# Kernel optimization log

Measured on AMD Instinct MI355X. Metric: run time of the kernel, lower is better.

Reference implementation:

```python
import jax, jax.numpy as jnp
import numpy as np

B, N, C = 4, 2048, 768
H = 12
D = C // H  # head_dim = 64
SCALE = D ** -0.5


def setup_inputs() -> dict:
    key = jax.random.key(0)
    ks = jax.random.split(key, 9)
    x = jax.random.normal(ks[0], (B, N, C), dtype=jnp.float32)
    k_in = jax.random.normal(ks[1], (B, N, C), dtype=jnp.float32)
    v_in = jax.random.normal(ks[2], (B, N, C), dtype=jnp.float32)
    rel_pos_bias = jax.random.normal(ks[3], (H, N, N), dtype=jnp.float32)
    # learned params (nn.Linear stores weight [out, in]; y = x @ W.T + b)
    s = C ** -0.5
    Wq = jax.random.normal(ks[4], (C, C), dtype=jnp.float32) * s
    Wk = jax.random.normal(ks[5], (C, C), dtype=jnp.float32) * s
    Wv = jax.random.normal(ks[6], (C, C), dtype=jnp.float32) * s
    Wp = jax.random.normal(ks[7], (C, C), dtype=jnp.float32) * s
    bp = jax.random.normal(ks[8], (C,), dtype=jnp.float32) * 0.01
    return {"x": x, "k_in": k_in, "v_in": v_in, "rel_pos_bias": rel_pos_bias,
            "Wq": Wq, "Wk": Wk, "Wv": Wv, "Wp": Wp, "bp": bp}


def reference(x, k_in, v_in, rel_pos_bias, Wq, Wk, Wv, Wp, bp):
    # linear projections (no q/k/v bias since qkv_bias=False)
    q = jnp.einsum('bnc,dc->bnd', x, Wq)      # [B,N,C]
    k = jnp.einsum('bnc,dc->bnd', k_in, Wk)   # [B,Nk,C]
    v = jnp.einsum('bnc,dc->bnd', v_in, Wv)   # [B,Nv,C]
    # split heads -> [B,H,N,D]
    q = q.reshape(B, N, H, D).transpose(0, 2, 1, 3) * SCALE
    k = k.reshape(B, -1, H, D).transpose(0, 2, 1, 3)
    v = v.reshape(B, -1, H, D).transpose(0, 2, 1, 3)
    attn = jnp.einsum('bhnd,bhmd->bhnm', q, k)          # [B,H,N,Nk]
    attn = attn + rel_pos_bias[None]                    # additive rel-pos bias
    attn = jax.nn.softmax(attn, axis=-1)
    out = jnp.einsum('bhnm,bhmd->bhnd', attn, v)        # [B,H,N,D]
    out = out.transpose(0, 2, 1, 3).reshape(B, N, C)
    return jnp.einsum('bnc,dc->bnd', out, Wp) + bp
```

## Files before the change

### kernel.cpp

```cpp
#include <hip/hip_runtime.h>
#include <stdint.h>
#include <stddef.h>

#define B_ 4
#define N_ 2048
#define C_ 768
#define H_ 12
#define M_ (B_ * N_)

typedef __attribute__((ext_vector_type(8))) short bf16x8_t;
typedef __attribute__((ext_vector_type(4))) float f32x4_t;

__device__ __forceinline__ unsigned pack2_bf16(float f0, float f1) {
  unsigned u0 = __builtin_bit_cast(unsigned, f0) + 0x8000u;
  unsigned u1 = __builtin_bit_cast(unsigned, f1) + 0x8000u;
  return __builtin_amdgcn_perm(u1, u0, 0x07060302u);
}

__device__ __forceinline__ short f2bf(float f) {
  unsigned u = __builtin_bit_cast(unsigned, f);
  u = (u + 0x7FFFu + ((u >> 16) & 1u)) >> 16;
  return (short)u;
}
__device__ __forceinline__ short f2bf_fast(float f) {
  return (short)((__builtin_bit_cast(unsigned, f) + 0x8000u) >> 16);
}

__device__ __forceinline__ void gload_lds16(const short* g, const short* l) {
  __builtin_amdgcn_global_load_lds(
      (const __attribute__((address_space(1))) void*)g,
      (__attribute__((address_space(3))) void*)l, 16, 0, 0);
}

#define XV 1572864
#define WV 147456
__global__ __launch_bounds__(256) void cvt_all(
    const float* __restrict__ x, const float* __restrict__ kin, const float* __restrict__ vin,
    const float* __restrict__ wq, const float* __restrict__ wk, const float* __restrict__ wv,
    const float* __restrict__ wp,
    unsigned short* __restrict__ xb, unsigned short* __restrict__ kb, unsigned short* __restrict__ vb,
    unsigned short* __restrict__ wqb, unsigned short* __restrict__ wkb, unsigned short* __restrict__ wvb,
    unsigned short* __restrict__ wpb)
{
  int i = blockIdx.x * 256 + threadIdx.x;
  const float* s; unsigned short* d; int off;
  if      (i < XV)            { s = x;   d = xb;  off = i; }
  else if (i < 2 * XV)        { s = kin; d = kb;  off = i - XV; }
  else if (i < 3 * XV)        { s = vin; d = vb;  off = i - 2 * XV; }
  else if (i < 3 * XV + WV)   { s = wq;  d = wqb; off = i - 3 * XV; }
  else if (i < 3 * XV + 2*WV) { s = wk;  d = wkb; off = i - 3 * XV - WV; }
  else if (i < 3 * XV + 3*WV) { s = wv;  d = wvb; off = i - 3 * XV - 2 * WV; }
  else                        { s = wp;  d = wpb; off = i - 3 * XV - 3 * WV; }
  float4 v = ((const float4*)s)[off];
  uint2 p;
  p.x = pack2_bf16(v.x, v.y);
  p.y = pack2_bf16(v.z, v.w);
  ((uint2*)d)[off] = p;
}

__global__ __launch_bounds__(256) void proj_qkv(
    const short* __restrict__ xb, const short* __restrict__ kb, const short* __restrict__ vb,
    const short* __restrict__ wqb, const short* __restrict__ wkb, const short* __restrict__ wvb,
    short* __restrict__ q_ws, short* __restrict__ k_ws, short* __restrict__ vt_ws)
{
  const int z = blockIdx.z;
  const short* A = (z == 0) ? xb : (z == 1) ? kb : vb;
  const short* W = (z == 0) ? wqb : (z == 1) ? wkb : wvb;
  const int m0 = blockIdx.x * 128;
  const int n0 = blockIdx.y * 128;

  __shared__ __align__(16) short smem[128 * 136];
  short* As = smem;
  short* Bs = smem + 128 * 64;

  const int t = threadIdx.x;
  const int w = t >> 6, L = t & 63, L15 = L & 15, quad = L >> 4;
  const int wm = w & 1, wn = w >> 1;

  f32x4_t acc[4][4] = {};

  const short* ga = A + (size_t)(m0 + w * 32 + (L >> 3)) * C_ + (L & 7) * 8;
  const short* gb = W + (size_t)(n0 + w * 32 + (L >> 3)) * C_ + (L & 7) * 8;
  const short* la = As + (w * 32) * 64;
  const short* lb = Bs + (w * 32) * 64;

  for (int k0 = 0; k0 < C_; k0 += 64) {
    __syncthreads();
    #pragma unroll
    for (int i = 0; i < 4; ++i) {
      gload_lds16(ga + (size_t)i * 8 * C_ + k0, la + i * 512);
      gload_lds16(gb + (size_t)i * 8 * C_ + k0, lb + i * 512);
    }
    __syncthreads();
    #pragma unroll
    for (int kk = 0; kk < 2; ++kk) {
      bf16x8_t af[4], bf[4];
      #pragma unroll
      for (int mt = 0; mt < 4; ++mt)
        af[mt] = *(const bf16x8_t*)&As[(wm * 64 + mt * 16 + L15) * 64 + kk * 32 + quad * 8];
      #pragma unroll
      for (int nt = 0; nt < 4; ++nt)
        bf[nt] = *(const bf16x8_t*)&Bs[(wn * 64 + nt * 16 + L15) * 64 + kk * 32 + quad * 8];
      #pragma unroll
      for (int mt = 0; mt < 4; ++mt)
        #pragma unroll
        for (int nt = 0; nt < 4; ++nt)
          acc[mt][nt] = __builtin_amdgcn_mfma_f32_16x16x32_bf16(af[mt], bf[nt], acc[mt][nt], 0, 0, 0);
    }
  }

  if (z != 2) {
    short* outp = (z == 0) ? q_ws : k_ws;
    const float mul = (z == 0) ? 0.125f : 1.0f;
    #pragma unroll
    for (int mt = 0; mt < 4; ++mt) {
      const int m_base = m0 + wm * 64 + mt * 16 + quad * 4;
      #pragma unroll
      for (int nt = 0; nt < 4; ++nt) {
        const int c = n0 + wn * 64 + nt * 16 + L15;
        const int h = c >> 6, d = c & 63;
        #pragma unroll
        for (int r = 0; r < 4; ++r) {
          const int m = m_base + r;
          const int b = m >> 11, n = m & 2047;
          outp[((size_t)(b * H_ + h) * N_ + n) * 64 + d] = f2bf(acc[mt][nt][r] * mul);
        }
      }
    }
  } else {
    __syncthreads();
    #pragma unroll
    for (int mt = 0; mt < 4; ++mt) {
      const int ml = wm * 64 + mt * 16 + quad * 4;
      #pragma unroll
      for (int nt = 0; nt < 4; ++nt) {
        const int cl = wn * 64 + nt * 16 + L15;
        #pragma unroll
        for (int r = 0; r < 4; ++r)
          smem[cl * 136 + ml + r] = f2bf(acc[mt][nt][r]);
      }
    }
    __syncthreads();
    const int bb = m0 >> 11;
    const int nn0 = m0 & 2047;
    #pragma unroll
    for (int pp = 0; pp < 8; ++pp) {
      const int cl = pp * 16 + (t >> 4);
      const int mg = t & 15;
      const uint4 val = *(const uint4*)&smem[cl * 136 + mg * 8];
      const int cg = n0 + cl;
      *(uint4*)&vt_ws[(((size_t)(bb * H_ + (cg >> 6))) * 64 + (cg & 63)) * N_ + nn0 + mg * 8] = val;
    }
  }
}

__global__ __launch_bounds__(256, 3) void attn(
    const short* __restrict__ q_ws, const short* __restrict__ k_ws,
    const short* __restrict__ vt_ws, const float* __restrict__ rpb,
    short* __restrict__ attn_out)
{
  const int p  = blockIdx.x;
  const int lw = (p & 7) * 96 + (p >> 3);
  const int h  = lw >> 6;
  const int xl = lw & 63;
  const int b  = xl & 3;
  const int m0 = (xl >> 2) * 128;
  const int bh = b * H_ + h;

  __shared__ __align__(16) short Ks [2][64 * 64];
  __shared__ __align__(16) short Vts[2][64 * 64];
  __shared__ __align__(16) short Ps [4][32 * 64];

  const int t = threadIdx.x;
  const int w = t >> 6, L = t & 63, L15 = L & 15, quad = L >> 4;

  const short* qp  = q_ws  + ((size_t)bh * N_ + m0) * 64;
  const short* kp  = k_ws  + (size_t)bh * N_ * 64;
  const short* vtp = vt_ws + (size_t)bh * 64 * N_;
  const float* bpb = rpb + (size_t)h * N_ * N_;

  const int srow8 = L >> 3;
  const int scolS = ((L & 7) ^ srow8) * 8;
  const short* gk_base = kp  + (size_t)(w * 16 + srow8) * 64 + scolS;
  const short* gv_base = vtp + (size_t)(w * 16 + srow8) * N_ + scolS;

  bf16x8_t aq[2][2];
  #pragma unroll
  for (int mt = 0; mt < 2; ++mt)
    #pragma unroll
    for (int kk = 0; kk < 2; ++kk)
      aq[mt][kk] = *(const bf16x8_t*)(qp + (size_t)(w * 32 + mt * 16 + L15) * 64 + kk * 32 + quad * 8);

  const float* bq = bpb + (size_t)(m0 + w * 32 + quad * 4) * N_ + L15;

  f32x4_t o[2][4] = {};
  float psum[2][4] = {};
  float bias[2][4][4];

  #pragma unroll
  for (int i = 0; i < 2; ++i) {
    gload_lds16(gk_base + (size_t)i * 8 * 64, &Ks[0][w * 1024 + i * 512]);
    gload_lds16(gv_base + (size_t)i * 8 * N_, &Vts[0][w * 1024 + i * 512]);
  }
  #pragma unroll
  for (int mt = 0; mt < 2; ++mt)
    #pragma unroll
    for (int r = 0; r < 4; ++r)
      #pragma unroll
      for (int nt = 0; nt < 4; ++nt)
        bias[mt][nt][r] = bq[(size_t)(mt * 16 + r) * N_ + nt * 16];
  __syncthreads();

  for (int T = 0; T < 32; ++T) {
    const int cur = T & 1, nxt = cur ^ 1;

    if (T < 31) {
      const int kv1 = (T + 1) * 64;
      #pragma unroll
      for (int i = 0; i < 2; ++i) {
        gload_lds16(gk_base + (size_t)(kv1 + i * 8) * 64, &Ks[nxt][w * 1024 + i * 512]);
        gload_lds16(gv_base + (size_t)i * 8 * N_ + kv1,   &Vts[nxt][w * 1024 + i * 512]);
      }
    }

    f32x4_t s[2][4];
    __builtin_amdgcn_s_setprio(1);
    #pragma unroll
    for (int nt = 0; nt < 4; ++nt) {
      const int row = nt * 16 + L15;
      const char* kbp = (const char*)Ks[cur] + row * 128;
      const int sx = (row & 7) << 4;
      const bf16x8_t b0 = *(const bf16x8_t*)(kbp + ((quad * 16) ^ sx));
      const bf16x8_t b1 = *(const bf16x8_t*)(kbp + ((64 + quad * 16) ^ sx));
      #pragma unroll
      for (int mt = 0; mt < 2; ++mt) {
        f32x4_t sv = {bias[mt][nt][0], bias[mt][nt][1], bias[mt][nt][2], bias[mt][nt][3]};
        sv = __builtin_amdgcn_mfma_f32_16x16x32_bf16(aq[mt][0], b0, sv, 0, 0, 0);
        s[mt][nt] = __builtin_amdgcn_mfma_f32_16x16x32_bf16(aq[mt][1], b1, sv, 0, 0, 0);
      }
    }
    __builtin_amdgcn_s_setprio(0);

    if (T < 31) {
      const float* bqn = bq + (size_t)(T + 1) * 64;
      #pragma unroll
      for (int mt = 0; mt < 2; ++mt)
        #pragma unroll
        for (int r = 0; r < 4; ++r)
          #pragma unroll
          for (int nt = 0; nt < 4; ++nt)
            bias[mt][nt][r] = bqn[(size_t)(mt * 16 + r) * N_ + nt * 16];
    }

    #pragma unroll
    for (int mt = 0; mt < 2; ++mt)
      #pragma unroll
      for (int nt = 0; nt < 4; ++nt)
        #pragma unroll
        for (int r = 0; r < 4; ++r) {
          const float e = __expf(s[mt][nt][r]);
          psum[mt][r] += e;
          const int qrow = mt * 16 + quad * 4 + r;
          const int cb = (nt * 32 + L15 * 2) ^ ((qrow & 7) << 4);
          *(short*)((char*)Ps[w] + qrow * 128 + cb) = f2bf_fast(e);
        }

    __builtin_amdgcn_s_setprio(1);
    #pragma unroll
    for (int kk = 0; kk < 2; ++kk) {
      bf16x8_t pa[2];
      #pragma unroll
      for (int mt = 0; mt < 2; ++mt) {
        const int row = mt * 16 + L15;
        pa[mt] = *(const bf16x8_t*)((char*)Ps[w] + row * 128 +
                                    ((kk * 64 + quad * 16) ^ ((row & 7) << 4)));
      }
      #pragma unroll
      for (int nt = 0; nt < 4; ++nt) {
        const int row = nt * 16 + L15;
        const bf16x8_t vbf = *(const bf16x8_t*)((char*)Vts[cur] + row * 128 +
                                                ((kk * 64 + quad * 16) ^ ((row & 7) << 4)));
        #pragma unroll
        for (int mt = 0; mt < 2; ++mt)
          o[mt][nt] = __builtin_amdgcn_mfma_f32_16x16x32_bf16(pa[mt], vbf, o[mt][nt], 0, 0, 0);
      }
    }
    __builtin_amdgcn_s_setprio(0);

    __syncthreads();
  }

  #pragma unroll
  for (int mt = 0; mt < 2; ++mt)
    #pragma unroll
    for (int r = 0; r < 4; ++r) {
      float v = psum[mt][r];
      v += __shfl_xor(v, 1);
      v += __shfl_xor(v, 2);
      v += __shfl_xor(v, 4);
      v += __shfl_xor(v, 8);
      psum[mt][r] = 1.0f / v;
    }

  #pragma unroll
  for (int mt = 0; mt < 2; ++mt) {
    const int n_base = m0 + w * 32 + mt * 16 + quad * 4;
    #pragma unroll
    for (int nt = 0; nt < 4; ++nt)
      #pragma unroll
      for (int r = 0; r < 4; ++r) {
        const float v = o[mt][nt][r] * psum[mt][r];
        attn_out[((size_t)(b * N_ + n_base + r)) * C_ + h * 64 + nt * 16 + L15] = f2bf(v);
      }
  }
}

__global__ __launch_bounds__(256) void proj_out(
    const short* __restrict__ Abf, const short* __restrict__ wpb,
    const float* __restrict__ bpv, float* __restrict__ out)
{
  const int m0 = blockIdx.x * 128;
  const int n0 = blockIdx.y * 128;

  __shared__ short As[128 * 64];
  __shared__ short Bs[128 * 64];

  const int t = threadIdx.x;
  const int w = t >> 6, L = t & 63, L15 = L & 15, quad = L >> 4;
  const int wm = w & 1, wn = w >> 1;

  f32x4_t acc[4][4] = {};

  const short* ga = Abf + (size_t)(m0 + w * 32 + (L >> 3)) * C_ + (L & 7) * 8;
  const short* gb = wpb + (size_t)(n0 + w * 32 + (L >> 3)) * C_ + (L & 7) * 8;
  const short* la = &As[(w * 32) * 64];
  const short* lb = &Bs[(w * 32) * 64];

  for (int k0 = 0; k0 < C_; k0 += 64) {
    __syncthreads();
    #pragma unroll
    for (int i = 0; i < 4; ++i) {
      gload_lds16(ga + (size_t)i * 8 * C_ + k0, la + i * 512);
      gload_lds16(gb + (size_t)i * 8 * C_ + k0, lb + i * 512);
    }
    __syncthreads();
    #pragma unroll
    for (int kk = 0; kk < 2; ++kk) {
      bf16x8_t af[4], bf[4];
      #pragma unroll
      for (int mt = 0; mt < 4; ++mt)
        af[mt] = *(const bf16x8_t*)&As[(wm * 64 + mt * 16 + L15) * 64 + kk * 32 + quad * 8];
      #pragma unroll
      for (int nt = 0; nt < 4; ++nt)
        bf[nt] = *(const bf16x8_t*)&Bs[(wn * 64 + nt * 16 + L15) * 64 + kk * 32 + quad * 8];
      #pragma unroll
      for (int mt = 0; mt < 4; ++mt)
        #pragma unroll
        for (int nt = 0; nt < 4; ++nt)
          acc[mt][nt] = __builtin_amdgcn_mfma_f32_16x16x32_bf16(af[mt], bf[nt], acc[mt][nt], 0, 0, 0);
    }
  }

  #pragma unroll
  for (int mt = 0; mt < 4; ++mt) {
    const int m_base = m0 + wm * 64 + mt * 16 + quad * 4;
    #pragma unroll
    for (int nt = 0; nt < 4; ++nt) {
      const int c = n0 + wn * 64 + nt * 16 + L15;
      const float bb = bpv[c];
      #pragma unroll
      for (int r = 0; r < 4; ++r)
        out[(size_t)(m_base + r) * C_ + c] = acc[mt][nt][r] + bb;
    }
  }
}

extern "C" void kernel_launch(void* const* d_in, const int* in_sizes, int n_in,
                              void* d_out, int out_size, void* d_ws, size_t ws_size,
                              hipStream_t stream) {
  const float* x    = (const float*)d_in[0];
  const float* k_in = (const float*)d_in[1];
  const float* v_in = (const float*)d_in[2];
  const float* rpb  = (const float*)d_in[3];
  const float* Wq   = (const float*)d_in[4];
  const float* Wk   = (const float*)d_in[5];
  const float* Wv   = (const float*)d_in[6];
  const float* Wp   = (const float*)d_in[7];
  const float* bp   = (const float*)d_in[8];
  float* out = (float*)d_out;

  const size_t SZ = (size_t)B_ * H_ * N_ * 64 * sizeof(short);
  const size_t WSZ = (size_t)C_ * C_ * sizeof(short);
  char* ws = (char*)d_ws;
  short* q_ws  = (short*)(ws);
  short* k_ws  = (short*)(ws + SZ);
  short* vt_ws = (short*)(ws + 2 * SZ);
  short* ao_ws = (short*)(ws + 3 * SZ);
  short* xb    = (short*)(ws + 4 * SZ);
  short* kb    = (short*)(ws + 5 * SZ);
  short* vb    = (short*)(ws + 6 * SZ);
  short* wqb   = (short*)(ws + 7 * SZ);
  short* wkb   = (short*)(ws + 7 * SZ + WSZ);
  short* wvb   = (short*)(ws + 7 * SZ + 2 * WSZ);
  short* wpb   = (short*)(ws + 7 * SZ + 3 * WSZ);

  cvt_all<<<(3 * XV + 4 * WV + 255) / 256, 256, 0, stream>>>(
      x, k_in, v_in, Wq, Wk, Wv, Wp,
      (unsigned short*)xb, (unsigned short*)kb, (unsigned short*)vb,
      (unsigned short*)wqb, (unsigned short*)wkb, (unsigned short*)wvb, (unsigned short*)wpb);
  proj_qkv<<<dim3(M_ / 128, C_ / 128, 3), 256, 0, stream>>>(
      xb, kb, vb, wqb, wkb, wvb, q_ws, k_ws, vt_ws);
  attn<<<dim3(B_ * (N_ / 128) * H_), 256, 0, stream>>>(q_ws, k_ws, vt_ws, rpb, ao_ws);
  proj_out<<<dim3(M_ / 128, C_ / 128), 256, 0, stream>>>(ao_ws, wpb, bp, out);
}
```

Before: 465.7 us.

## Compute transposed S tile so bias loads and P stores vectorize

Result: slower. 483.3 us (+3.8%).

```diff
diff --git a/kernel.cpp b/kernel.cpp
--- a/kernel.cpp
+++ b/kernel.cpp
@@ -21,9 +21,6 @@
   unsigned u = __builtin_bit_cast(unsigned, f);
   u = (u + 0x7FFFu + ((u >> 16) & 1u)) >> 16;
   return (short)u;
-}
-__device__ __forceinline__ short f2bf_fast(float f) {
-  return (short)((__builtin_bit_cast(unsigned, f) + 0x8000u) >> 16);
 }
 
 __device__ __forceinline__ void gload_lds16(const short* g, const short* l) {
@@ -191,11 +188,11 @@
     for (int kk = 0; kk < 2; ++kk)
       aq[mt][kk] = *(const bf16x8_t*)(qp + (size_t)(w * 32 + mt * 16 + L15) * 64 + kk * 32 + quad * 8);
 
-  const float* bq = bpb + (size_t)(m0 + w * 32 + quad * 4) * N_ + L15;
+  const float* bq = bpb + (size_t)(m0 + w * 32 + L15) * N_ + quad * 4;
 
   f32x4_t o[2][4] = {};
-  float psum[2][4] = {};
-  float bias[2][4][4];
+  float psum[2] = {0.0f, 0.0f};
+  f32x4_t bias[2][4];
 
   #pragma unroll
   for (int i = 0; i < 2; ++i) {
@@ -205,10 +202,8 @@
   #pragma unroll
   for (int mt = 0; mt < 2; ++mt)
     #pragma unroll
-    for (int r = 0; r < 4; ++r)
-      #pragma unroll
-      for (int nt = 0; nt < 4; ++nt)
-        bias[mt][nt][r] = bq[(size_t)(mt * 16 + r) * N_ + nt * 16];
+    for (int nt = 0; nt < 4; ++nt)
+      bias[mt][nt] = *(const f32x4_t*)(bq + (size_t)mt * 16 * N_ + nt * 16);
   __syncthreads();
 
   for (int T = 0; T < 32; ++T) {
@@ -230,13 +225,13 @@
       const int row = nt * 16 + L15;
       const char* kbp = (const char*)Ks[cur] + row * 128;
       const int sx = (row & 7) << 4;
-      const bf16x8_t b0 = *(const bf16x8_t*)(kbp + ((quad * 16) ^ sx));
-      const bf16x8_t b1 = *(const bf16x8_t*)(kbp + ((64 + quad * 16) ^ sx));
+      const bf16x8_t k0 = *(const bf16x8_t*)(kbp + ((quad * 16) ^ sx));
+      const bf16x8_t k1 = *(const bf16x8_t*)(kbp + ((64 + quad * 16) ^ sx));
       #pragma unroll
       for (int mt = 0; mt < 2; ++mt) {
-        f32x4_t sv = {bias[mt][nt][0], bias[mt][nt][1], bias[mt][nt][2], bias[mt][nt][3]};
-        sv = __builtin_amdgcn_mfma_f32_16x16x32_bf16(aq[mt][0], b0, sv, 0, 0, 0);
-        s[mt][nt] = __builtin_amdgcn_mfma_f32_16x16x32_bf16(aq[mt][1], b1, sv, 0, 0, 0);
+        f32x4_t sv = bias[mt][nt];
+        sv = __builtin_amdgcn_mfma_f32_16x16x32_bf16(k0, aq[mt][0], sv, 0, 0, 0);
+        s[mt][nt] = __builtin_amdgcn_mfma_f32_16x16x32_bf16(k1, aq[mt][1], sv, 0, 0, 0);
       }
     }
     __builtin_amdgcn_s_setprio(0);
@@ -246,24 +241,28 @@
       #pragma unroll
       for (int mt = 0; mt < 2; ++mt)
         #pragma unroll
-        for (int r = 0; r < 4; ++r)
-          #pragma unroll
-          for (int nt = 0; nt < 4; ++nt)
-            bias[mt][nt][r] = bqn[(size_t)(mt * 16 + r) * N_ + nt * 16];
-    }
-
-    #pragma unroll
-    for (int mt = 0; mt < 2; ++mt)
-      #pragma unroll
-      for (int nt = 0; nt < 4; ++nt)
-        #pragma unroll
-        for (int r = 0; r < 4; ++r) {
-          const float e = __expf(s[mt][nt][r]);
-          psum[mt][r] += e;
-          const int qrow = mt * 16 + quad * 4 + r;
-          const int cb = (nt * 32 + L15 * 2) ^ ((qrow & 7) << 4);
-          *(short*)((char*)Ps[w] + qrow * 128 + cb) = f2bf_fast(e);
-        }
+        for (int nt = 0; nt < 4; ++nt)
+          bias[mt][nt] = *(const f32x4_t*)(bqn + (size_t)mt * 16 * N_ + nt * 16);
+    }
+
+    #pragma unroll
+    for (int mt = 0; mt < 2; ++mt) {
+      const int qrow = mt * 16 + L15;
+      const int swz = (qrow & 7) << 4;
+      #pragma unroll
+      for (int nt = 0; nt < 4; ++nt) {
+        const float e0 = __expf(s[mt][nt][0]);
+        const float e1 = __expf(s[mt][nt][1]);
+        const float e2 = __expf(s[mt][nt][2]);
+        const float e3 = __expf(s[mt][nt][3]);
+        psum[mt] += (e0 + e1) + (e2 + e3);
+        uint2 pk;
+        pk.x = pack2_bf16(e0, e1);
+        pk.y = pack2_bf16(e2, e3);
+        const int cb = (nt * 32 + quad * 8) ^ swz;
+        *(uint2*)((char*)Ps[w] + qrow * 128 + cb) = pk;
+      }
+    }
 
     __builtin_amdgcn_s_setprio(1);
     #pragma unroll
@@ -290,26 +289,27 @@
     __syncthreads();
   }
 
-  #pragma unroll
-  for (int mt = 0; mt < 2; ++mt)
-    #pragma unroll
-    for (int r = 0; r < 4; ++r) {
-      float v = psum[mt][r];
-      v += __shfl_xor(v, 1);
-      v += __shfl_xor(v, 2);
-      v += __shfl_xor(v, 4);
-      v += __shfl_xor(v, 8);
-      psum[mt][r] = 1.0f / v;
-    }
+  float inv[2];
+  #pragma unroll
+  for (int mt = 0; mt < 2; ++mt) {
+    float v = psum[mt];
+    v += __shfl_xor(v, 16);
+    v += __shfl_xor(v, 32);
+    inv[mt] = v;
+  }
 
   #pragma unroll
   for (int mt = 0; mt < 2; ++mt) {
     const int n_base = m0 + w * 32 + mt * 16 + quad * 4;
+    float rl[4];
+    #pragma unroll
+    for (int r = 0; r < 4; ++r)
+      rl[r] = 1.0f / __shfl(inv[mt], quad * 4 + r);
     #pragma unroll
     for (int nt = 0; nt < 4; ++nt)
       #pragma unroll
       for (int r = 0; r < 4; ++r) {
-        const float v = o[mt][nt][r] * psum[mt][r];
+        const float v = o[mt][nt][r] * rl[r];
         attn_out[((size_t)(b * N_ + n_base + r)) * C_ + h * 64 + nt * 16 + L15] = f2bf(v);
       }
   }
```

## Double-buffer LDS tiles in projection GEMMs to overlap loads with MFMA

Applied to the files above, without the earlier changes.

Result: no change. 457.0 us (-1.9%).

```diff
diff --git a/kernel.cpp b/kernel.cpp
--- a/kernel.cpp
+++ b/kernel.cpp
@@ -69,9 +69,7 @@
   const int m0 = blockIdx.x * 128;
   const int n0 = blockIdx.y * 128;
 
-  __shared__ __align__(16) short smem[128 * 136];
-  short* As = smem;
-  short* Bs = smem + 128 * 64;
+  __shared__ __align__(16) short smem[2 * 16384];
 
   const int t = threadIdx.x;
   const int w = t >> 6, L = t & 63, L15 = L & 15, quad = L >> 4;
@@ -81,32 +79,47 @@
 
   const short* ga = A + (size_t)(m0 + w * 32 + (L >> 3)) * C_ + (L & 7) * 8;
   const short* gb = W + (size_t)(n0 + w * 32 + (L >> 3)) * C_ + (L & 7) * 8;
-  const short* la = As + (w * 32) * 64;
-  const short* lb = Bs + (w * 32) * 64;
-
-  for (int k0 = 0; k0 < C_; k0 += 64) {
-    __syncthreads();
-    #pragma unroll
-    for (int i = 0; i < 4; ++i) {
-      gload_lds16(ga + (size_t)i * 8 * C_ + k0, la + i * 512);
-      gload_lds16(gb + (size_t)i * 8 * C_ + k0, lb + i * 512);
-    }
-    __syncthreads();
+  const int lofs = (w * 32) * 64;
+
+  #pragma unroll
+  for (int i = 0; i < 4; ++i) {
+    gload_lds16(ga + (size_t)i * 8 * C_, smem + lofs + i * 512);
+    gload_lds16(gb + (size_t)i * 8 * C_, smem + 8192 + lofs + i * 512);
+  }
+  __syncthreads();
+
+  for (int T = 0; T < 12; ++T) {
+    const int cur = T & 1;
+    const short* Acur = smem + cur * 16384;
+    const short* Bcur = Acur + 8192;
+
+    if (T < 11) {
+      short* Anxt = smem + (cur ^ 1) * 16384;
+      const int k1 = (T + 1) * 64;
+      #pragma unroll
+      for (int i = 0; i < 4; ++i) {
+        gload_lds16(ga + (size_t)i * 8 * C_ + k1, Anxt + lofs + i * 512);
+        gload_lds16(gb + (size_t)i * 8 * C_ + k1, Anxt + 8192 + lofs + i * 512);
+      }
+    }
+
     #pragma unroll
     for (int kk = 0; kk < 2; ++kk) {
       bf16x8_t af[4], bf[4];
       #pragma unroll
       for (int mt = 0; mt < 4; ++mt)
-        af[mt] = *(const bf16x8_t*)&As[(wm * 64 + mt * 16 + L15) * 64 + kk * 32 + quad * 8];
+        af[mt] = *(const bf16x8_t*)&Acur[(wm * 64 + mt * 16 + L15) * 64 + kk * 32 + quad * 8];
       #pragma unroll
       for (int nt = 0; nt < 4; ++nt)
-        bf[nt] = *(const bf16x8_t*)&Bs[(wn * 64 + nt * 16 + L15) * 64 + kk * 32 + quad * 8];
+        bf[nt] = *(const bf16x8_t*)&Bcur[(wn * 64 + nt * 16 + L15) * 64 + kk * 32 + quad * 8];
       #pragma unroll
       for (int mt = 0; mt < 4; ++mt)
         #pragma unroll
         for (int nt = 0; nt < 4; ++nt)
           acc[mt][nt] = __builtin_amdgcn_mfma_f32_16x16x32_bf16(af[mt], bf[nt], acc[mt][nt], 0, 0, 0);
     }
+
+    __syncthreads();
   }
 
   if (z != 2) {
@@ -128,7 +141,6 @@
       }
     }
   } else {
-    __syncthreads();
     #pragma unroll
     for (int mt = 0; mt < 4; ++mt) {
       const int ml = wm * 64 + mt * 16 + quad * 4;
@@ -322,8 +334,7 @@
   const int m0 = blockIdx.x * 128;
   const int n0 = blockIdx.y * 128;
 
-  __shared__ short As[128 * 64];
-  __shared__ short Bs[128 * 64];
+  __shared__ __align__(16) short smem[2 * 16384];
 
   const int t = threadIdx.x;
   const int w = t >> 6, L = t & 63, L15 = L & 15, quad = L >> 4;
@@ -333,32 +344,47 @@
 
   const short* ga = Abf + (size_t)(m0 + w * 32 + (L >> 3)) * C_ + (L & 7) * 8;
   const short* gb = wpb + (size_t)(n0 + w * 32 + (L >> 3)) * C_ + (L & 7) * 8;
-  const short* la = &As[(w * 32) * 64];
-  const short* lb = &Bs[(w * 32) * 64];
-
-  for (int k0 = 0; k0 < C_; k0 += 64) {
-    __syncthreads();
-    #pragma unroll
-    for (int i = 0; i < 4; ++i) {
-      gload_lds16(ga + (size_t)i * 8 * C_ + k0, la + i * 512);
-      gload_lds16(gb + (size_t)i * 8 * C_ + k0, lb + i * 512);
-    }
-    __syncthreads();
+  const int lofs = (w * 32) * 64;
+
+  #pragma unroll
+  for (int i = 0; i < 4; ++i) {
+    gload_lds16(ga + (size_t)i * 8 * C_, smem + lofs + i * 512);
+    gload_lds16(gb + (size_t)i * 8 * C_, smem + 8192 + lofs + i * 512);
+  }
+  __syncthreads();
+
+  for (int T = 0; T < 12; ++T) {
+    const int cur = T & 1;
+    const short* Acur = smem + cur * 16384;
+    const short* Bcur = Acur + 8192;
+
+    if (T < 11) {
+      short* Anxt = smem + (cur ^ 1) * 16384;
+      const int k1 = (T + 1) * 64;
+      #pragma unroll
+      for (int i = 0; i < 4; ++i) {
+        gload_lds16(ga + (size_t)i * 8 * C_ + k1, Anxt + lofs + i * 512);
+        gload_lds16(gb + (size_t)i * 8 * C_ + k1, Anxt + 8192 + lofs + i * 512);
+      }
+    }
+
     #pragma unroll
     for (int kk = 0; kk < 2; ++kk) {
       bf16x8_t af[4], bf[4];
       #pragma unroll
       for (int mt = 0; mt < 4; ++mt)
-        af[mt] = *(const bf16x8_t*)&As[(wm * 64 + mt * 16 + L15) * 64 + kk * 32 + quad * 8];
+        af[mt] = *(const bf16x8_t*)&Acur[(wm * 64 + mt * 16 + L15) * 64 + kk * 32 + quad * 8];
       #pragma unroll
       for (int nt = 0; nt < 4; ++nt)
-        bf[nt] = *(const bf16x8_t*)&Bs[(wn * 64 + nt * 16 + L15) * 64 + kk * 32 + quad * 8];
+        bf[nt] = *(const bf16x8_t*)&Bcur[(wn * 64 + nt * 16 + L15) * 64 + kk * 32 + quad * 8];
       #pragma unroll
       for (int mt = 0; mt < 4; ++mt)
         #pragma unroll
         for (int nt = 0; nt < 4; ++nt)
           acc[mt][nt] = __builtin_amdgcn_mfma_f32_16x16x32_bf16(af[mt], bf[nt], acc[mt][nt], 0, 0, 0);
     }
+
+    __syncthreads();
   }
 
   #pragma unroll
```
